# Performance work log

Hardware: AMD Instinct MI355X
Metric: run time of the kernel (lower is better)

## Reference

```python
import jax, jax.numpy as jnp
import numpy as np

D_MODEL = 1024
NUM_HEADS = 16
B, S = 4, 2048


def setup_inputs() -> dict:
    key = jax.random.key(0)
    ks = jax.random.split(key, 9)
    sc = 1.0 / np.sqrt(D_MODEL)
    return {
        "inputs": jax.random.normal(ks[0], (B, S, D_MODEL), dtype=jnp.float32),
        "Wq": jax.random.normal(ks[1], (D_MODEL, D_MODEL), dtype=jnp.float32) * sc,
        "bq": jax.random.normal(ks[2], (D_MODEL,), dtype=jnp.float32) * 0.02,
        "Wk": jax.random.normal(ks[3], (D_MODEL, D_MODEL), dtype=jnp.float32) * sc,
        "bk": jax.random.normal(ks[4], (D_MODEL,), dtype=jnp.float32) * 0.02,
        "Wv": jax.random.normal(ks[5], (D_MODEL, D_MODEL), dtype=jnp.float32) * sc,
        "bv": jax.random.normal(ks[6], (D_MODEL,), dtype=jnp.float32) * 0.02,
        "Wo": jax.random.normal(ks[7], (D_MODEL, D_MODEL), dtype=jnp.float32) * sc,
        "bo": jax.random.normal(ks[8], (D_MODEL,), dtype=jnp.float32) * 0.02,
    }


def reference(inputs, Wq, bq, Wk, bk, Wv, bv, Wo, bo):
    H = NUM_HEADS
    b, s, d = inputs.shape
    hd = d // H  # head dim for q, k, v (all equal here)

    # Linear projections, then split into heads: [B, H, S, hd]
    def split_heads(x):
        return x.reshape(b, s, H, hd).transpose(0, 2, 1, 3)

    q = split_heads(inputs @ Wq + bq)
    k = split_heads(inputs @ Wk + bk)
    v = split_heads(inputs @ Wv + bv)

    # Scaled dot-product attention per head (batched over B, H)
    scores = jnp.einsum("bhqd,bhkd->bhqk", q, k) / jnp.sqrt(jnp.asarray(hd, dtype=q.dtype))
    causal = jnp.tril(jnp.ones((s, s), dtype=bool))
    scores = jnp.where(causal[None, None], scores, jnp.asarray(-jnp.inf, dtype=scores.dtype))
    attn = jax.nn.softmax(scores, axis=-1)
    ctx = jnp.einsum("bhqk,bhkd->bhqd", attn, v)  # [B, H, S, hd]

    # Concatenate heads and final projection
    concat = ctx.transpose(0, 2, 1, 3).reshape(b, s, d)
    return concat @ Wo + bo
```

## Files before the change

kernel.cpp:

```cpp
#include <hip/hip_runtime.h>
#include <hip/hip_bf16.h>
#include <math.h>

typedef __attribute__((ext_vector_type(8))) short short8;
typedef __attribute__((ext_vector_type(4))) float floatx4;
typedef __attribute__((ext_vector_type(16))) float floatx16;
typedef __attribute__((ext_vector_type(2))) int int2v;

#define D_MODEL 1024
#define NHEAD   16
#define HD      64
#define BATCH   4
#define SEQ     2048
#define M_TOT   (BATCH * SEQ)

__device__ __forceinline__ unsigned short f2bf(float f) {
  unsigned int u = __builtin_bit_cast(unsigned int, f);
  u += 0x7FFFu + ((u >> 16) & 1u);
  return (unsigned short)(u >> 16);
}

__device__ __forceinline__ unsigned pk2(float a, float b) {
  unsigned r;
  asm("v_cvt_pk_bf16_f32 %0, %1, %2" : "=v"(r) : "v"(a), "v"(b));
  return r;
}

__device__ __forceinline__ void gl_lds16(const void* g, void* l) {
  __builtin_amdgcn_global_load_lds((__attribute__((address_space(1))) void*)g,
                                   (__attribute__((address_space(3))) void*)l,
                                   16, 0, 0);
}

__device__ __forceinline__ int aswz(int r) { return (r ^ (r >> 3)) & 7; }

__global__ __launch_bounds__(256) void cvt_x_kernel(const float* __restrict__ X,
                                                    unsigned short* __restrict__ Xb) {
  int i = blockIdx.x * 256 + threadIdx.x;
  float4 v = reinterpret_cast<const float4*>(X)[i];
  ushort4 o;
  o.x = f2bf(v.x); o.y = f2bf(v.y); o.z = f2bf(v.z); o.w = f2bf(v.w);
  reinterpret_cast<ushort4*>(Xb)[i] = o;
}

__global__ __launch_bounds__(256) void cvt_wt_kernel(const float* __restrict__ W0,
                                                     const float* __restrict__ W1,
                                                     const float* __restrict__ W2,
                                                     const float* __restrict__ W3,
                                                     unsigned short* __restrict__ T0,
                                                     unsigned short* __restrict__ T1,
                                                     unsigned short* __restrict__ T2,
                                                     unsigned short* __restrict__ T3) {
  const float* W;
  unsigned short* T;
  switch (blockIdx.z) {
    case 0: W = W0; T = T0; break;
    case 1: W = W1; T = T1; break;
    case 2: W = W2; T = T2; break;
    default: W = W3; T = T3; break;
  }
  __shared__ unsigned short tile[64][65];
  int n0 = blockIdx.x * 64, k0 = blockIdx.y * 64;
#pragma unroll
  for (int i = 0; i < 16; ++i) {
    int e = threadIdx.x + i * 256;
    int r = e >> 6, c = e & 63;
    tile[r][c] = f2bf(W[(size_t)(k0 + r) * D_MODEL + n0 + c]);
  }
  __syncthreads();
#pragma unroll
  for (int i = 0; i < 16; ++i) {
    int e = threadIdx.x + i * 256;
    int r = e >> 6, c = e & 63;
    T[(size_t)(n0 + r) * D_MODEL + k0 + c] = tile[c][r];
  }
}

__global__ __launch_bounds__(256) void qkv_gemm_kernel(
    const unsigned short* __restrict__ Xb,
    const unsigned short* __restrict__ WqT, const unsigned short* __restrict__ WkT,
    const unsigned short* __restrict__ WvT,
    const float* __restrict__ bq, const float* __restrict__ bk, const float* __restrict__ bv,
    unsigned short* __restrict__ Qo, unsigned short* __restrict__ Ko,
    unsigned short* __restrict__ Vo) {
  const unsigned short* Bt;
  const float* bias;
  unsigned short* Out;
  float scale;
  if (blockIdx.z == 0)      { Bt = WqT; bias = bq; Out = Qo; scale = 0.18033688f; }
  else if (blockIdx.z == 1) { Bt = WkT; bias = bk; Out = Ko; scale = 1.0f; }
  else                      { Bt = WvT; bias = bv; Out = Vo; scale = 1.0f; }

  __shared__ unsigned short As[128 * 64];
  __shared__ unsigned short Bs[128 * 64];

  int m0 = blockIdx.x * 128, n0 = blockIdx.y * 128;
  int tid = threadIdx.x;
  int lane = tid & 63;
  int w = tid >> 6;
  int wr = (w >> 1) * 64, wc = (w & 1) * 64;
  int l15 = lane & 15, lg = lane >> 4;
  int lr8 = lane >> 3, lc8 = lane & 7;

  floatx4 acc[4][4];
#pragma unroll
  for (int mi = 0; mi < 4; ++mi)
#pragma unroll
    for (int ni = 0; ni < 4; ++ni)
#pragma unroll
      for (int e = 0; e < 4; ++e) acc[mi][ni][e] = 0.0f;

  for (int kt = 0; kt < D_MODEL / 64; ++kt) {
    int k0 = kt * 64;
#pragma unroll
    for (int i = 0; i < 4; ++i) {
      int c = w + i * 4;
      int r = c * 8 + lr8;
      int blk = lc8 ^ (r & 7);
      gl_lds16(&Xb[(size_t)(m0 + r) * D_MODEL + k0 + blk * 8], &As[c * 512]);
      gl_lds16(&Bt[(size_t)(n0 + r) * D_MODEL + k0 + blk * 8], &Bs[c * 512]);
    }
    __syncthreads();
#pragma unroll
    for (int kk = 0; kk < 2; ++kk) {
      short8 af[4], bf[4];
#pragma unroll
      for (int mi = 0; mi < 4; ++mi) {
        int row = wr + mi * 16 + l15;
        int col = (kk * 32 + lg * 8) ^ ((row & 7) << 3);
        af[mi] = *reinterpret_cast<const short8*>(&As[row * 64 + col]);
      }
#pragma unroll
      for (int ni = 0; ni < 4; ++ni) {
        int row = wc + ni * 16 + l15;
        int col = (kk * 32 + lg * 8) ^ ((row & 7) << 3);
        bf[ni] = *reinterpret_cast<const short8*>(&Bs[row * 64 + col]);
      }
#pragma unroll
      for (int mi = 0; mi < 4; ++mi)
#pragma unroll
        for (int ni = 0; ni < 4; ++ni)
          acc[mi][ni] =
              __builtin_amdgcn_mfma_f32_16x16x32_bf16(af[mi], bf[ni], acc[mi][ni], 0, 0, 0);
    }
    __syncthreads();
  }

  bool vout = (blockIdx.z == 2);
#pragma unroll
  for (int mi = 0; mi < 4; ++mi)
#pragma unroll
    for (int ni = 0; ni < 4; ++ni) {
      int n = n0 + wc + ni * 16 + l15;
      float bia = bias[n];
      int h = n >> 6, d = n & 63;
#pragma unroll
      for (int r = 0; r < 4; ++r) {
        int m = m0 + wr + mi * 16 + lg * 4 + r;
        int b = m >> 11, s = m & 2047;
        float val = (acc[mi][ni][r] + bia) * scale;
        size_t idx;
        if (vout)
          idx = (((size_t)(b * NHEAD + h)) * HD + d) * SEQ + s;
        else
          idx = (((size_t)(b * NHEAD + h)) * SEQ + s) * HD + d;
        Out[idx] = f2bf(val);
      }
    }
}

__global__ __launch_bounds__(256) void attn_kernel(const unsigned short* __restrict__ Q,
                                                   const unsigned short* __restrict__ K,
                                                   const unsigned short* __restrict__ Vt,
                                                   unsigned short* __restrict__ ctx) {
  __shared__ unsigned short Ks[2][64 * 64];
  __shared__ unsigned short Vs[2][64 * 64];

  int bh = blockIdx.y;
  int tid = threadIdx.x;
  int lane = tid & 63;
  int w = tid >> 6;
  int l31 = lane & 31;
  int hi = lane >> 5;
  int lr8 = lane >> 3, lc8 = lane & 7;

  const unsigned short* Qb = Q + (size_t)bh * SEQ * HD;
  const unsigned short* Kb = K + (size_t)bh * SEQ * HD;
  const unsigned short* Vb = Vt + (size_t)bh * HD * SEQ;
  int b = bh >> 4, h = bh & 15;

  for (int ph = 0; ph < 2; ++ph) {
    int qt = (ph == 0) ? (int)blockIdx.x : 15 - (int)blockIdx.x;
    int q0 = qt * 128;
    int myq = q0 + w * 32 + l31;

    short8 qf[4];
#pragma unroll
    for (int kc = 0; kc < 4; ++kc)
      qf[kc] = *reinterpret_cast<const short8*>(&Qb[(size_t)myq * HD + kc * 16 + hi * 8]);

    floatx16 oacc[2];
#pragma unroll
    for (int db = 0; db < 2; ++db)
#pragma unroll
      for (int r = 0; r < 16; ++r) oacc[db][r] = 0.0f;
    float lrow = 0.0f;

    int nt = 2 * qt + 2;

#pragma unroll
    for (int i = 0; i < 2; ++i) {
      int c = w + i * 4;
      int r = c * 8 + lr8;
      int blk = lc8 ^ aswz(r);
      gl_lds16(&Kb[(size_t)r * HD + blk * 8], &Ks[0][c * 512]);
      gl_lds16(&Vb[(size_t)r * SEQ + blk * 8], &Vs[0][c * 512]);
    }
    __syncthreads();

    for (int t = 0; t < nt; ++t) {
      int buf = t & 1;
      if (t + 1 < nt) {
        int kb1 = (t + 1) * 64;
        const unsigned short* kg = Kb + (size_t)kb1 * HD;
        const unsigned short* vg = Vb + kb1;
#pragma unroll
        for (int i = 0; i < 2; ++i) {
          int c = w + i * 4;
          int r = c * 8 + lr8;
          int blk = lc8 ^ aswz(r);
          gl_lds16(&kg[(size_t)r * HD + blk * 8], &Ks[buf ^ 1][c * 512]);
          gl_lds16(&vg[(size_t)r * SEQ + blk * 8], &Vs[buf ^ 1][c * 512]);
        }
      }

      floatx16 sfT[2];
#pragma unroll
      for (int kb = 0; kb < 2; ++kb) {
#pragma unroll
        for (int r = 0; r < 16; ++r) sfT[kb][r] = 0.0f;
#pragma unroll
        for (int kc = 0; kc < 4; ++kc) {
          int row = kb * 32 + l31;
          int col = (kc * 16 + hi * 8) ^ (aswz(row) << 3);
          short8 kf = *reinterpret_cast<const short8*>(&Ks[buf][row * 64 + col]);
          sfT[kb] = __builtin_amdgcn_mfma_f32_32x32x16_bf16(kf, qf[kc], sfT[kb], 0, 0, 0);
        }
      }

      if (t >= nt - 2) {
        int kb0 = t * 64;
#pragma unroll
        for (int kb = 0; kb < 2; ++kb)
#pragma unroll
          for (int r = 0; r < 16; ++r) {
            int key = kb0 + kb * 32 + (r & 3) + 8 * (r >> 2) + 4 * hi;
            if (key > myq) sfT[kb][r] = -INFINITY;
          }
      }

      float ts0 = 0.0f, ts1 = 0.0f, ts2 = 0.0f, ts3 = 0.0f;
#pragma unroll
      for (int kb = 0; kb < 2; ++kb)
#pragma unroll
        for (int r = 0; r < 16; r += 4) {
          float p0 = exp2f(sfT[kb][r]);
          float p1 = exp2f(sfT[kb][r + 1]);
          float p2 = exp2f(sfT[kb][r + 2]);
          float p3 = exp2f(sfT[kb][r + 3]);
          sfT[kb][r] = p0; sfT[kb][r + 1] = p1;
          sfT[kb][r + 2] = p2; sfT[kb][r + 3] = p3;
          ts0 += p0; ts1 += p1; ts2 += p2; ts3 += p3;
        }
      float ts = (ts0 + ts1) + (ts2 + ts3);
      ts += __shfl_xor(ts, 32);
      lrow += ts;

#pragma unroll
      for (int kb = 0; kb < 2; ++kb) {
        unsigned D[8];
#pragma unroll
        for (int m = 0; m < 8; ++m) D[m] = pk2(sfT[kb][2 * m], sfT[kb][2 * m + 1]);
#pragma unroll
        for (int c = 0; c < 2; ++c) {
          int2v r0 = __builtin_amdgcn_permlane32_swap((int)D[4 * c], (int)D[4 * c + 2], false, false);
          int2v r1 = __builtin_amdgcn_permlane32_swap((int)D[4 * c + 1], (int)D[4 * c + 3], false, false);
          uint4 u;
          u.x = (unsigned)r0[0];
          u.y = (unsigned)r1[0];
          u.z = (unsigned)r0[1];
          u.w = (unsigned)r1[1];
          short8 pa = __builtin_bit_cast(short8, u);
          int kc = kb * 2 + c;
#pragma unroll
          for (int db = 0; db < 2; ++db) {
            int row = db * 32 + l31;
            int col = (kc * 16 + hi * 8) ^ (aswz(row) << 3);
            short8 vf = *reinterpret_cast<const short8*>(&Vs[buf][row * 64 + col]);
            oacc[db] = __builtin_amdgcn_mfma_f32_32x32x16_bf16(pa, vf, oacc[db], 0, 0, 0);
          }
        }
      }
      __syncthreads();
    }

    int base32 = lane & 32;
    float lrowD[16];
#pragma unroll
    for (int r = 0; r < 16; ++r) {
      int q31 = (r & 3) + 8 * (r >> 2) + 4 * hi;
      lrowD[r] = __shfl(lrow, base32 + q31);
    }
#pragma unroll
    for (int db = 0; db < 2; ++db) {
      int d = db * 32 + l31;
#pragma unroll
      for (int r = 0; r < 16; ++r) {
        int qr = q0 + w * 32 + (r & 3) + 8 * (r >> 2) + 4 * hi;
        float val = oacc[db][r] / lrowD[r];
        ctx[((size_t)(b * SEQ + qr)) * D_MODEL + h * HD + d] = f2bf(val);
      }
    }
    __syncthreads();
  }
}

__global__ __launch_bounds__(256) void out_gemm_kernel(const unsigned short* __restrict__ A,
                                                       const unsigned short* __restrict__ Bt,
                                                       const float* __restrict__ bias,
                                                       float* __restrict__ Out) {
  __shared__ unsigned short As[128 * 64];
  __shared__ unsigned short Bs[128 * 64];

  int m0 = blockIdx.x * 128, n0 = blockIdx.y * 128;
  int tid = threadIdx.x;
  int lane = tid & 63;
  int w = tid >> 6;
  int wr = (w >> 1) * 64, wc = (w & 1) * 64;
  int l15 = lane & 15, lg = lane >> 4;
  int lr8 = lane >> 3, lc8 = lane & 7;

  floatx4 acc[4][4];
#pragma unroll
  for (int mi = 0; mi < 4; ++mi)
#pragma unroll
    for (int ni = 0; ni < 4; ++ni)
#pragma unroll
      for (int e = 0; e < 4; ++e) acc[mi][ni][e] = 0.0f;

  for (int kt = 0; kt < D_MODEL / 64; ++kt) {
    int k0 = kt * 64;
#pragma unroll
    for (int i = 0; i < 4; ++i) {
      int c = w + i * 4;
      int r = c * 8 + lr8;
      int blk = lc8 ^ (r & 7);
      gl_lds16(&A[(size_t)(m0 + r) * D_MODEL + k0 + blk * 8], &As[c * 512]);
      gl_lds16(&Bt[(size_t)(n0 + r) * D_MODEL + k0 + blk * 8], &Bs[c * 512]);
    }
    __syncthreads();
#pragma unroll
    for (int kk = 0; kk < 2; ++kk) {
      short8 af[4], bf[4];
#pragma unroll
      for (int mi = 0; mi < 4; ++mi) {
        int row = wr + mi * 16 + l15;
        int col = (kk * 32 + lg * 8) ^ ((row & 7) << 3);
        af[mi] = *reinterpret_cast<const short8*>(&As[row * 64 + col]);
      }
#pragma unroll
      for (int ni = 0; ni < 4; ++ni) {
        int row = wc + ni * 16 + l15;
        int col = (kk * 32 + lg * 8) ^ ((row & 7) << 3);
        bf[ni] = *reinterpret_cast<const short8*>(&Bs[row * 64 + col]);
      }
#pragma unroll
      for (int mi = 0; mi < 4; ++mi)
#pragma unroll
        for (int ni = 0; ni < 4; ++ni)
          acc[mi][ni] =
              __builtin_amdgcn_mfma_f32_16x16x32_bf16(af[mi], bf[ni], acc[mi][ni], 0, 0, 0);
    }
    __syncthreads();
  }

#pragma unroll
  for (int mi = 0; mi < 4; ++mi)
#pragma unroll
    for (int ni = 0; ni < 4; ++ni) {
      int n = n0 + wc + ni * 16 + l15;
      float bia = bias[n];
#pragma unroll
      for (int r = 0; r < 4; ++r) {
        int m = m0 + wr + mi * 16 + lg * 4 + r;
        Out[(size_t)m * D_MODEL + n] = acc[mi][ni][r] + bia;
      }
    }
}

extern "C" void kernel_launch(void* const* d_in, const int* in_sizes, int n_in,
                              void* d_out, int out_size, void* d_ws, size_t ws_size,
                              hipStream_t stream) {
  const float* X  = (const float*)d_in[0];
  const float* Wq = (const float*)d_in[1];
  const float* bq = (const float*)d_in[2];
  const float* Wk = (const float*)d_in[3];
  const float* bk = (const float*)d_in[4];
  const float* Wv = (const float*)d_in[5];
  const float* bv = (const float*)d_in[6];
  const float* Wo = (const float*)d_in[7];
  const float* bo = (const float*)d_in[8];
  float* out = (float*)d_out;

  char* ws = (char*)d_ws;
  const size_t MB = 1024 * 1024;
  unsigned short* Xb   = (unsigned short*)(ws);
  unsigned short* WqT  = (unsigned short*)(ws + 16 * MB);
  unsigned short* WkT  = (unsigned short*)(ws + 18 * MB);
  unsigned short* WvT  = (unsigned short*)(ws + 20 * MB);
  unsigned short* WoT  = (unsigned short*)(ws + 22 * MB);
  unsigned short* Qw   = (unsigned short*)(ws + 24 * MB);
  unsigned short* Kw   = (unsigned short*)(ws + 40 * MB);
  unsigned short* Vtw  = (unsigned short*)(ws + 56 * MB);
  unsigned short* Ctx  = (unsigned short*)(ws + 72 * MB);

  cvt_x_kernel<<<(M_TOT * D_MODEL / 4) / 256, 256, 0, stream>>>(X, Xb);
  cvt_wt_kernel<<<dim3(16, 16, 4), 256, 0, stream>>>(Wq, Wk, Wv, Wo, WqT, WkT, WvT, WoT);
  qkv_gemm_kernel<<<dim3(M_TOT / 128, D_MODEL / 128, 3), 256, 0, stream>>>(
      Xb, WqT, WkT, WvT, bq, bk, bv, Qw, Kw, Vtw);
  attn_kernel<<<dim3(8, BATCH * NHEAD), 256, 0, stream>>>(Qw, Kw, Vtw, Ctx);
  out_gemm_kernel<<<dim3(M_TOT / 128, D_MODEL / 128), 256, 0, stream>>>(Ctx, WoT, bo, out);
}
```

Before: 287.5 us.

## Use 128-key tiles in attention with per-warp diagonal skipping

Doubles the K/V tile staged per iteration from 64 to 128 keys, halving the number of loop iterations and the barriers between them. V gets a new 128-wide swizzled shared-memory layout. On the diagonal tile each warp computes only the key blocks up to its own query rows, skipping fully masked MFMAs and exps. In exchange, shared memory doubles to 64KB per block, which may reduce occupancy, and the per-warp early skip adds divergent control flow across warps.

```diff
diff --git a/kernel.cpp b/kernel.cpp
--- a/kernel.cpp
+++ b/kernel.cpp
@@ -173,8 +173,8 @@
                                                    const unsigned short* __restrict__ K,
                                                    const unsigned short* __restrict__ Vt,
                                                    unsigned short* __restrict__ ctx) {
-  __shared__ unsigned short Ks[2][64 * 64];
-  __shared__ unsigned short Vs[2][64 * 64];
+  __shared__ unsigned short Ks[2][128 * 64];
+  __shared__ unsigned short Vs[2][64 * 128];
 
   int bh = blockIdx.y;
   int tid = threadIdx.x;
@@ -183,6 +183,7 @@
   int l31 = lane & 31;
   int hi = lane >> 5;
   int lr8 = lane >> 3, lc8 = lane & 7;
+  int lr16 = lane >> 4, lc16 = lane & 15;
 
   const unsigned short* Qb = Q + (size_t)bh * SEQ * HD;
   const unsigned short* Kb = K + (size_t)bh * SEQ * HD;
@@ -206,37 +207,36 @@
       for (int r = 0; r < 16; ++r) oacc[db][r] = 0.0f;
     float lrow = 0.0f;
 
-    int nt = 2 * qt + 2;
-
-#pragma unroll
-    for (int i = 0; i < 2; ++i) {
-      int c = w + i * 4;
-      int r = c * 8 + lr8;
-      int blk = lc8 ^ aswz(r);
-      gl_lds16(&Kb[(size_t)r * HD + blk * 8], &Ks[0][c * 512]);
-      gl_lds16(&Vb[(size_t)r * SEQ + blk * 8], &Vs[0][c * 512]);
-    }
+    int nt = qt + 1;
+
+    auto stage = [&](int bufi, int t) {
+      int kb0 = t * 128;
+#pragma unroll
+      for (int i = 0; i < 4; ++i) {
+        int c = w + i * 4;
+        int rk = c * 8 + lr8;
+        int gk = lc8 ^ aswz(rk);
+        gl_lds16(&Kb[(size_t)(kb0 + rk) * HD + gk * 8], &Ks[bufi][c * 512]);
+        int rv = c * 4 + lr16;
+        int gv = lc16 ^ (rv & 15);
+        gl_lds16(&Vb[(size_t)rv * SEQ + kb0 + gv * 8], &Vs[bufi][c * 512]);
+      }
+    };
+
+    stage(0, 0);
     __syncthreads();
 
     for (int t = 0; t < nt; ++t) {
       int buf = t & 1;
-      if (t + 1 < nt) {
-        int kb1 = (t + 1) * 64;
-        const unsigned short* kg = Kb + (size_t)kb1 * HD;
-        const unsigned short* vg = Vb + kb1;
-#pragma unroll
-        for (int i = 0; i < 2; ++i) {
-          int c = w + i * 4;
-          int r = c * 8 + lr8;
-          int blk = lc8 ^ aswz(r);
-          gl_lds16(&kg[(size_t)r * HD + blk * 8], &Ks[buf ^ 1][c * 512]);
-          gl_lds16(&vg[(size_t)r * SEQ + blk * 8], &Vs[buf ^ 1][c * 512]);
-        }
-      }
-
-      floatx16 sfT[2];
-#pragma unroll
-      for (int kb = 0; kb < 2; ++kb) {
+      if (t + 1 < nt) stage(buf ^ 1, t + 1);
+
+      bool diag = (t == nt - 1);
+      int wlim = diag ? w : 3;
+
+      floatx16 sfT[4];
+#pragma unroll
+      for (int kb = 0; kb < 4; ++kb) {
+        if (kb > wlim) continue;
 #pragma unroll
         for (int r = 0; r < 16; ++r) sfT[kb][r] = 0.0f;
 #pragma unroll
@@ -248,20 +248,18 @@
         }
       }
 
-      if (t >= nt - 2) {
-        int kb0 = t * 64;
-#pragma unroll
-        for (int kb = 0; kb < 2; ++kb)
-#pragma unroll
-          for (int r = 0; r < 16; ++r) {
-            int key = kb0 + kb * 32 + (r & 3) + 8 * (r >> 2) + 4 * hi;
-            if (key > myq) sfT[kb][r] = -INFINITY;
-          }
+      if (diag) {
+#pragma unroll
+        for (int r = 0; r < 16; ++r) {
+          int key = q0 + w * 32 + (r & 3) + 8 * (r >> 2) + 4 * hi;
+          if (key > myq) sfT[w][r] = -INFINITY;
+        }
       }
 
       float ts0 = 0.0f, ts1 = 0.0f, ts2 = 0.0f, ts3 = 0.0f;
 #pragma unroll
-      for (int kb = 0; kb < 2; ++kb)
+      for (int kb = 0; kb < 4; ++kb) {
+        if (kb > wlim) continue;
 #pragma unroll
         for (int r = 0; r < 16; r += 4) {
           float p0 = exp2f(sfT[kb][r]);
@@ -272,12 +270,14 @@
           sfT[kb][r + 2] = p2; sfT[kb][r + 3] = p3;
           ts0 += p0; ts1 += p1; ts2 += p2; ts3 += p3;
         }
+      }
       float ts = (ts0 + ts1) + (ts2 + ts3);
       ts += __shfl_xor(ts, 32);
       lrow += ts;
 
 #pragma unroll
-      for (int kb = 0; kb < 2; ++kb) {
+      for (int kb = 0; kb < 4; ++kb) {
+        if (kb > wlim) continue;
         unsigned D[8];
 #pragma unroll
         for (int m = 0; m < 8; ++m) D[m] = pk2(sfT[kb][2 * m], sfT[kb][2 * m + 1]);
@@ -295,8 +295,8 @@
 #pragma unroll
           for (int db = 0; db < 2; ++db) {
             int row = db * 32 + l31;
-            int col = (kc * 16 + hi * 8) ^ (aswz(row) << 3);
-            short8 vf = *reinterpret_cast<const short8*>(&Vs[buf][row * 64 + col]);
+            int col = (kc * 16 + hi * 8) ^ ((row & 15) << 3);
+            short8 vf = *reinterpret_cast<const short8*>(&Vs[buf][row * 128 + col]);
             oacc[db] = __builtin_amdgcn_mfma_f32_32x32x16_bf16(pa, vf, oacc[db], 0, 0, 0);
           }
         }
```

Result: slower. 360.7 us (+25.5%).
